# Optimization experiments

Measured on AMD Instinct MI355X. Metric: run time of the kernel, lower is better.

## Reference

```python
import jax, jax.numpy as jnp
import numpy as np

WH, WW = 7, 7           # window height/width
N = WH * WW             # tokens per window = 49
C = 768                 # num_channels
H = 24                  # num_heads
D = C // H              # head_dim = 32
B = 1024                # total windows (batch * windows-per-image)
NW = 64                 # windows per image (shift_mask leading dim)
EPS = 1e-5


def _relative_position_index():
    # Mirrors the torch buffer construction in __init__.
    coords = np.stack(np.meshgrid(np.arange(WH), np.arange(WW), indexing='ij'))  # [2,WH,WW]
    cf = coords.reshape(2, -1)                          # [2,N]
    rel = cf[:, :, None] - cf[:, None, :]               # [2,N,N]
    rel = rel.transpose(1, 2, 0).copy()                 # [N,N,2]
    rel[:, :, 0] += WH - 1
    rel[:, :, 1] += WW - 1
    rel[:, :, 0] *= 2 * WW - 1
    return jnp.asarray(rel.sum(-1), dtype=jnp.int32)    # [N,N]


def setup_inputs() -> dict:
    key = jax.random.key(0)
    ks = jax.random.split(key, 6)
    x = jax.random.normal(ks[0], (B, N, C), dtype=jnp.float32)
    shift_mask = jax.random.normal(ks[1], (NW, N, N), dtype=jnp.float32)
    w_qkv = jax.random.normal(ks[2], (3 * C, C), dtype=jnp.float32) * 0.02
    b_qkv = jnp.zeros((3 * C,), dtype=jnp.float32)
    w_proj = jax.random.normal(ks[3], (C, C), dtype=jnp.float32) * 0.02
    b_proj = jnp.zeros((C,), dtype=jnp.float32)
    rel_bias_table = jax.random.normal(ks[4], ((2 * WH - 1) * (2 * WW - 1), H), dtype=jnp.float32) * 0.02
    ln_g = jnp.ones((C,), dtype=jnp.float32)
    ln_b = jnp.zeros((C,), dtype=jnp.float32)
    rel_pos_index = _relative_position_index()
    return {
        'x': x, 'shift_mask': shift_mask,
        'w_qkv': w_qkv, 'b_qkv': b_qkv,
        'w_proj': w_proj, 'b_proj': b_proj,
        'rel_bias_table': rel_bias_table,
        'ln_g': ln_g, 'ln_b': ln_b,
        'rel_pos_index': rel_pos_index,
    }


def reference(x, shift_mask, w_qkv, b_qkv, w_proj, b_proj, rel_bias_table, ln_g, ln_b, rel_pos_index):
    B_, N_, C_ = x.shape
    # QKV projection: [B,N,3C] -> [3,B,H,N,D]
    qkv = (x @ w_qkv.T + b_qkv).reshape(B_, N_, 3, H, D).transpose(2, 0, 3, 1, 4)
    q, k, v = qkv[0], qkv[1], qkv[2]
    # Relative position bias gather: [N,N,H] -> [1,H,N,N]
    bias = rel_bias_table[rel_pos_index.reshape(-1)].reshape(N_, N_, H).transpose(2, 0, 1)[None]
    # Shift mask broadcast over batch repeats and heads: [B,1,N,N]
    mask = jnp.tile(shift_mask, (B_ // shift_mask.shape[0], 1, 1))[:, None]
    attn_bias = bias + mask  # [B,H,N,N]
    scale = 1.0 / np.sqrt(D).astype(np.float32)
    scores = jnp.einsum('bhnd,bhmd->bhnm', q, k) * scale + attn_bias
    attn = jax.nn.softmax(scores, axis=-1)
    out = jnp.einsum('bhnm,bhmd->bhnd', attn, v)       # [B,H,N,D]
    out = out.transpose(0, 2, 1, 3).reshape(B_, N_, C_)
    out = out @ w_proj.T + b_proj                      # dropout p=0 -> identity
    y = out + x
    mu = jnp.mean(y, axis=-1, keepdims=True)
    var = jnp.mean(jnp.square(y - mu), axis=-1, keepdims=True)
    return (y - mu) * jax.lax.rsqrt(var + EPS) * ln_g + ln_b
```

## Files before the change

### kernel.cpp

```cpp
#include <hip/hip_runtime.h>
#include <hip/hip_bf16.h>

#define SEQ 49
#define CH 768
#define NH 24
#define HD 32
#define NB 1024
#define NWIN 64
#define MTOT (NB*SEQ)

typedef __hip_bfloat16 bf16;
typedef __attribute__((ext_vector_type(8))) short short8;
typedef __attribute__((ext_vector_type(4))) short short4v;
typedef __attribute__((ext_vector_type(4))) float f32x4;

#define MD  ((size_t)MTOT * HD)
#define NHMD ((size_t)NH * MD)

__device__ __forceinline__ void gload16(const void* g, void* l) {
  __builtin_amdgcn_global_load_lds((__attribute__((address_space(1))) void*)g,
                                   (__attribute__((address_space(3))) void*)l,
                                   16, 0, 0);
}

__device__ __forceinline__ float bf2f(short s) {
  return __uint_as_float(((unsigned int)(unsigned short)s) << 16);
}

__global__ void cvt_bf16(const float* __restrict__ in, bf16* __restrict__ o, int n4) {
  int i = blockIdx.x * blockDim.x + threadIdx.x;
  if (i >= n4) return;
  float4 v = ((const float4*)in)[i];
  union { bf16 b[4]; short4 s; } u;
  u.b[0] = __float2bfloat16(v.x);
  u.b[1] = __float2bfloat16(v.y);
  u.b[2] = __float2bfloat16(v.z);
  u.b[3] = __float2bfloat16(v.w);
  ((short4*)o)[i] = u.s;
}

__global__ void build_comb(const float* __restrict__ table, const int* __restrict__ rpi,
                           const float* __restrict__ smask, bf16* __restrict__ comb) {
  int i = blockIdx.x * blockDim.x + threadIdx.x;
  if (i >= NWIN * NH * 1024) return;
  int idx = i * 4;
  int e0 = idx & 7;
  int l = (idx >> 3) & 63;
  int jj = (idx >> 9) & 7;
  int sh = idx >> 12;
  int h = sh % NH;
  int s = sh / NH;
  union { bf16 b[4]; short4 v; } u;
#pragma unroll
  for (int k = 0; k < 4; k++) {
    int j = jj * 8 + e0 + k;
    int mt = j >> 4, nt = (j >> 2) & 3, r = j & 3;
    int m = 16 * mt + 4 * (l >> 4) + r;
    int n = 16 * nt + (l & 15);
    float v = -1e30f;
    if (m < SEQ && n < SEQ)
      v = (table[rpi[m * SEQ + n] * NH + h] + smask[s * SEQ * SEQ + m * SEQ + n])
          * 1.4426950408889634f;
    u.b[k] = __float2bfloat16(v);
  }
  *(short4*)(comb + idx) = u.v;
}

__global__ __launch_bounds__(512) void qkv_gemm(
    const bf16* __restrict__ A, const bf16* __restrict__ Bw,
    const float* __restrict__ bias, bf16* __restrict__ C)
{
  extern __shared__ __align__(16) bf16 lds[];
  const int tid = threadIdx.x;
  const int w = tid >> 6, l = tid & 63;
  const int lr = l & 15, lg = l >> 4;
  const int wm = w >> 2, wn = w & 3;

  const int flat = blockIdx.x;
  const int xcd = flat & 7, lid = flat >> 3;
  const int wgid = (xcd < 4 ? xcd * 221 : 884 + (xcd - 4) * 220) + lid;
  const int bm = wgid / 9, bn = wgid - 9 * bm;

  const bf16* gA[4];
  const bf16* gB[4];
  int ldst[4];
#pragma unroll
  for (int j = 0; j < 4; j++) {
    int c = j * 512 + tid;
    int row = c >> 3, cpos = c & 7;
    int srcch = cpos ^ (row & 7);
    gA[j] = A + ((size_t)(bm * 256 + row)) * CH + srcch * 8;
    gB[j] = Bw + ((size_t)(bn * 256 + row)) * CH + srcch * 8;
    ldst[j] = c * 8;
  }

  f32x4 acc[8][4];
  f32x4 zero4 = {0.f, 0.f, 0.f, 0.f};
#pragma unroll
  for (int i = 0; i < 8; i++)
#pragma unroll
    for (int j = 0; j < 4; j++) acc[i][j] = zero4;

  int offA[8][2], offB[4][2];
#pragma unroll
  for (int mi = 0; mi < 8; mi++)
#pragma unroll
    for (int ks = 0; ks < 2; ks++) {
      int rowa = wm * 128 + mi * 16 + lr;
      offA[mi][ks] = rowa * 64 + ((lg + 4 * ks) ^ (rowa & 7)) * 8;
    }
#pragma unroll
  for (int nj = 0; nj < 4; nj++)
#pragma unroll
    for (int ks = 0; ks < 2; ks++) {
      int rowb = wn * 64 + nj * 16 + lr;
      offB[nj][ks] = rowb * 64 + ((lg + 4 * ks) ^ (rowb & 7)) * 8;
    }

#pragma unroll
  for (int j = 0; j < 4; j++) gload16(gA[j], lds + ldst[j]);
#pragma unroll
  for (int j = 0; j < 4; j++) gload16(gB[j], lds + 32768 + ldst[j]);

  for (int t = 0; t < 12; ++t) {
    const int cur = t & 1;
    asm volatile("s_waitcnt vmcnt(0)" ::: "memory");
    __builtin_amdgcn_sched_barrier(0);
    __builtin_amdgcn_s_barrier();
    __builtin_amdgcn_sched_barrier(0);
    const bf16* cA = lds + cur * 16384;
    const bf16* cB = lds + 32768 + cur * 16384;
    bf16* nA = lds + (cur ^ 1) * 16384;
    bf16* nB = lds + 32768 + (cur ^ 1) * 16384;
    const int kk = (t + 1) * 64;
    const bool pf = (t < 11);
#pragma unroll
    for (int ks = 0; ks < 2; ks++) {
      short8 bfv[4];
#pragma unroll
      for (int nj = 0; nj < 4; nj++) bfv[nj] = *(const short8*)(cB + offB[nj][ks]);
#pragma unroll
      for (int hp = 0; hp < 2; hp++) {
        short8 af[4];
#pragma unroll
        for (int mi = 0; mi < 4; mi++) af[mi] = *(const short8*)(cA + offA[hp * 4 + mi][ks]);
        if (pf) {
          const int j = ks * 2 + hp;
          gload16(gA[j] + kk, nA + ldst[j]);
          gload16(gB[j] + kk, nB + ldst[j]);
        }
        asm volatile("s_waitcnt lgkmcnt(0)" ::: "memory");
        __builtin_amdgcn_sched_barrier(0);
        __builtin_amdgcn_s_setprio(1);
#pragma unroll
        for (int mi = 0; mi < 4; mi++)
#pragma unroll
          for (int nj = 0; nj < 4; nj++)
            acc[hp * 4 + mi][nj] =
                __builtin_amdgcn_mfma_f32_16x16x32_bf16(af[mi], bfv[nj], acc[hp * 4 + mi][nj], 0, 0, 0);
        __builtin_amdgcn_s_setprio(0);
      }
    }
  }

  const float scale = 0.25503487724583985f;
  const int colbase = bn * 256 + 64 * wn;
  const int rowbase = bm * 256 + 128 * wm;
#pragma unroll
  for (int nj = 0; nj < 4; nj++) {
    const int cb16 = colbase + 16 * nj;
    const int sec = cb16 / 768;
    const int rem = cb16 - sec * 768;
    const int h = rem >> 5;
    const int dbase = rem & 31;
    float bv = bias[cb16 + lr];
    if (sec == 2) {
      const size_t vbase = 2 * NHMD + ((size_t)h * HD + dbase + lr) * MTOT;
#pragma unroll
      for (int mi = 0; mi < 8; mi++) {
        size_t row = rowbase + 16 * mi + 4 * lg;
        union { bf16 b[4]; short4 s; } u;
#pragma unroll
        for (int r = 0; r < 4; r++) u.b[r] = __float2bfloat16(acc[mi][nj][r] + bv);
        *(short4*)(C + vbase + row) = u.s;
      }
    } else {
      const float mul = (sec == 0) ? scale : 1.0f;
      const size_t base = (size_t)sec * NHMD + (size_t)h * MD + dbase + lr;
#pragma unroll
      for (int mi = 0; mi < 8; mi++) {
#pragma unroll
        for (int r = 0; r < 4; r++) {
          size_t row = rowbase + 16 * mi + 4 * lg + r;
          C[base + row * HD] = __float2bfloat16((acc[mi][nj][r] + bv) * mul);
        }
      }
    }
  }
}

__global__ __launch_bounds__(256, 3) void attn_kernel(
    const bf16* __restrict__ qkvT, const bf16* __restrict__ comb,
    bf16* __restrict__ aout)
{
  __shared__ __align__(16) bf16 P[4][64 * 72];
  const int tid = threadIdx.x;
  const int w = tid >> 6, l = tid & 63;
  const int lr = l & 15, lg = l >> 4;
  const int b = blockIdx.x;
  const int h = blockIdx.y * 4 + w;
  const size_t rowb = (size_t)b * SEQ;
  f32x4 zero4 = {0.f, 0.f, 0.f, 0.f};

  const bf16* qb = qkvT + (size_t)h * MD + rowb * HD;
  const bf16* kb = qkvT + NHMD + (size_t)h * MD + rowb * HD;
  const bf16* vT = qkvT + 2 * NHMD + (size_t)h * HD * MTOT;

  short8 qf[4], kf[4];
#pragma unroll
  for (int mt = 0; mt < 4; mt++)
    qf[mt] = *(const short8*)(qb + (16 * mt + lr) * HD + 8 * lg);
#pragma unroll
  for (int nt = 0; nt < 4; nt++)
    kf[nt] = *(const short8*)(kb + (16 * nt + lr) * HD + 8 * lg);

  f32x4 s[4][4];
#pragma unroll
  for (int mt = 0; mt < 4; mt++)
#pragma unroll
    for (int nt = 0; nt < 4; nt++)
      s[mt][nt] = __builtin_amdgcn_mfma_f32_16x16x32_bf16(qf[mt], kf[nt], zero4, 0, 0, 0);

  short8 pb[2][2];
#pragma unroll
  for (int kt = 0; kt < 2; kt++)
#pragma unroll
    for (int dt = 0; dt < 2; dt++)
      pb[kt][dt] = *(const short8*)(vT + ((size_t)(16 * dt + lr)) * MTOT + rowb + 32 * kt + 8 * lg);

  const bf16* cbp = comb + (((size_t)(b & (NWIN - 1)) * NH + h) << 12);
  short8 c8[8];
#pragma unroll
  for (int jj = 0; jj < 8; jj++)
    c8[jj] = *(const short8*)(cbp + (jj * 64 + l) * 8);
#pragma unroll
  for (int jj = 0; jj < 8; jj++)
#pragma unroll
    for (int e = 0; e < 8; e++)
      s[jj >> 1][(jj & 1) * 2 + (e >> 2)][e & 3] += bf2f(c8[jj][e]);

  float inv[4][4];
#pragma unroll
  for (int mt = 0; mt < 4; mt++)
#pragma unroll
    for (int r = 0; r < 4; r++) {
      float t = 0.f;
#pragma unroll
      for (int nt = 0; nt < 4; nt++) {
        float e = exp2f(s[mt][nt][r]);
        s[mt][nt][r] = e;
        t += e;
      }
      t += __shfl_xor(t, 1, 64);
      t += __shfl_xor(t, 2, 64);
      t += __shfl_xor(t, 4, 64);
      t += __shfl_xor(t, 8, 64);
      inv[mt][r] = 1.0f / t;
    }

#pragma unroll
  for (int mt = 0; mt < 4; mt++)
#pragma unroll
    for (int nt = 0; nt < 4; nt++)
#pragma unroll
      for (int r = 0; r < 4; r++)
        P[w][(16 * mt + 4 * lg + r) * 72 + 16 * nt + lr] =
            __float2bfloat16(s[mt][nt][r]);

  f32x4 o[4][2];
#pragma unroll
  for (int mt = 0; mt < 4; mt++) { o[mt][0] = zero4; o[mt][1] = zero4; }
#pragma unroll
  for (int kt = 0; kt < 2; kt++) {
    short8 pa[4];
#pragma unroll
    for (int mt = 0; mt < 4; mt++)
      pa[mt] = *(const short8*)(&P[w][(16 * mt + lr) * 72 + 32 * kt + 8 * lg]);
#pragma unroll
    for (int mt = 0; mt < 4; mt++)
#pragma unroll
      for (int dt = 0; dt < 2; dt++)
        o[mt][dt] = __builtin_amdgcn_mfma_f32_16x16x32_bf16(pa[mt], pb[kt][dt], o[mt][dt], 0, 0, 0);
  }

#pragma unroll
  for (int mt = 0; mt < 4; mt++)
#pragma unroll
    for (int dt = 0; dt < 2; dt++)
#pragma unroll
      for (int r = 0; r < 4; r++) {
        int m = 16 * mt + 4 * lg + r;
        if (m < SEQ)
          aout[(rowb + m) * CH + h * HD + 16 * dt + lr] =
              __float2bfloat16(o[mt][dt][r] * inv[mt][r]);
      }
}

__global__ __launch_bounds__(256) void proj_gemm(
    const bf16* __restrict__ A, const bf16* __restrict__ Bw,
    const float* __restrict__ bias, const bf16* __restrict__ xb,
    bf16* __restrict__ Y)
{
  __shared__ __align__(16) bf16 As[2 * 128 * 64];
  __shared__ __align__(16) bf16 Bs[2 * 128 * 64];
  const int tid = threadIdx.x;
  const int w = tid >> 6, l = tid & 63;
  const int lr = l & 15, lg = l >> 4;
  const int wm = w >> 1, wn = w & 1;

  const int flat = blockIdx.x;
  const int wg = (flat & 7) * 294 + (flat >> 3);
  const int bm = wg / 6, bn = wg - 6 * (wg / 6);

  const bf16* gA[4];
  const bf16* gB[4];
  int ldst[4];
#pragma unroll
  for (int j = 0; j < 4; j++) {
    int c = j * 256 + tid;
    int row = c >> 3, cpos = c & 7;
    int srcch = cpos ^ (row & 7);
    gA[j] = A + ((size_t)(bm * 128 + row)) * CH + srcch * 8;
    gB[j] = Bw + ((size_t)(bn * 128 + row)) * CH + srcch * 8;
    ldst[j] = c * 8;
  }

  f32x4 acc[4][4];
  f32x4 zero4 = {0.f, 0.f, 0.f, 0.f};
#pragma unroll
  for (int i = 0; i < 4; i++)
#pragma unroll
    for (int j = 0; j < 4; j++) acc[i][j] = zero4;

  int offA[4][2], offB[4][2];
#pragma unroll
  for (int mi = 0; mi < 4; mi++) {
#pragma unroll
    for (int ks = 0; ks < 2; ks++) {
      int rowa = 64 * wm + 16 * mi + lr;
      offA[mi][ks] = rowa * 64 + ((lg + 4 * ks) ^ (rowa & 7)) * 8;
      int rowb = 64 * wn + 16 * mi + lr;
      offB[mi][ks] = rowb * 64 + ((lg + 4 * ks) ^ (rowb & 7)) * 8;
    }
  }

#pragma unroll
  for (int j = 0; j < 4; j++) gload16(gA[j], As + ldst[j]);
#pragma unroll
  for (int j = 0; j < 4; j++) gload16(gB[j], Bs + ldst[j]);

  for (int t = 0; t < 12; ++t) {
    const int base = (t & 1) * 8192;
    asm volatile("s_waitcnt vmcnt(0)" ::: "memory");
    __builtin_amdgcn_sched_barrier(0);
    __builtin_amdgcn_s_barrier();
    __builtin_amdgcn_sched_barrier(0);
    const bf16* cA = As + base;
    const bf16* cB = Bs + base;
    bf16* nA = As + (base ^ 8192);
    bf16* nB = Bs + (base ^ 8192);
    const int kk = (t + 1) * 64;
    const bool pf = (t < 11);
#pragma unroll
    for (int ks = 0; ks < 2; ks++) {
      short8 af[4], bfv[4];
#pragma unroll
      for (int mi = 0; mi < 4; mi++) {
        af[mi] = *(const short8*)(cA + offA[mi][ks]);
        bfv[mi] = *(const short8*)(cB + offB[mi][ks]);
      }
      if (pf) {
#pragma unroll
        for (int j = 0; j < 2; j++) {
          gload16(gA[ks * 2 + j] + kk, nA + ldst[ks * 2 + j]);
          gload16(gB[ks * 2 + j] + kk, nB + ldst[ks * 2 + j]);
        }
      }
      asm volatile("s_waitcnt lgkmcnt(0)" ::: "memory");
      __builtin_amdgcn_sched_barrier(0);
      __builtin_amdgcn_s_setprio(1);
#pragma unroll
      for (int mi = 0; mi < 4; mi++)
#pragma unroll
        for (int nj = 0; nj < 4; nj++)
          acc[mi][nj] = __builtin_amdgcn_mfma_f32_16x16x32_bf16(af[mi], bfv[nj], acc[mi][nj], 0, 0, 0);
      __builtin_amdgcn_s_setprio(0);
    }
  }

  const int colbase = bn * 128 + 64 * wn;
  const int rowbase = bm * 128 + 64 * wm;
#pragma unroll
  for (int nj = 0; nj < 4; nj++) {
    int col = colbase + 16 * nj + lr;
    float bv = bias[col];
#pragma unroll
    for (int mi = 0; mi < 4; mi++) {
#pragma unroll
      for (int r = 0; r < 4; r++) {
        size_t row = rowbase + 16 * mi + 4 * lg + r;
        float v = acc[mi][nj][r] + bv + bf2f(((const short*)xb)[row * CH + col]);
        Y[row * CH + col] = __float2bfloat16(v);
      }
    }
  }
}

__global__ __launch_bounds__(256) void ln_kernel(
    const bf16* __restrict__ Y, const float* __restrict__ g,
    const float* __restrict__ be, float* __restrict__ out)
{
  const int w = threadIdx.x >> 6, l = threadIdx.x & 63;
  const size_t r = (size_t)blockIdx.x * 4 + w;
  const bf16* yr = Y + r * CH;

  short8 a = *(const short8*)(yr + 8 * l);
  short4v b4 = *(const short4v*)(yr + 512 + 4 * l);
  float v[12];
#pragma unroll
  for (int j = 0; j < 8; j++) v[j] = bf2f(a[j]);
#pragma unroll
  for (int j = 0; j < 4; j++) v[8 + j] = bf2f(b4[j]);

  float s1 = 0.f, s2 = 0.f;
#pragma unroll
  for (int j = 0; j < 12; j++) { s1 += v[j]; s2 += v[j] * v[j]; }
#pragma unroll
  for (int m = 1; m <= 32; m <<= 1) {
    s1 += __shfl_xor(s1, m, 64);
    s2 += __shfl_xor(s2, m, 64);
  }
  float mu = s1 * (1.0f / 768.0f);
  float var = s2 * (1.0f / 768.0f) - mu * mu;
  float rs = rsqrtf(var + 1e-5f);

  float4 g0 = *(const float4*)(g + 8 * l);
  float4 g1 = *(const float4*)(g + 8 * l + 4);
  float4 g2 = *(const float4*)(g + 512 + 4 * l);
  float4 b0 = *(const float4*)(be + 8 * l);
  float4 b1 = *(const float4*)(be + 8 * l + 4);
  float4 b2 = *(const float4*)(be + 512 + 4 * l);

  float4 o0, o1, o2;
  o0.x = (v[0] - mu) * rs * g0.x + b0.x;
  o0.y = (v[1] - mu) * rs * g0.y + b0.y;
  o0.z = (v[2] - mu) * rs * g0.z + b0.z;
  o0.w = (v[3] - mu) * rs * g0.w + b0.w;
  o1.x = (v[4] - mu) * rs * g1.x + b1.x;
  o1.y = (v[5] - mu) * rs * g1.y + b1.y;
  o1.z = (v[6] - mu) * rs * g1.z + b1.z;
  o1.w = (v[7] - mu) * rs * g1.w + b1.w;
  o2.x = (v[8] - mu) * rs * g2.x + b2.x;
  o2.y = (v[9] - mu) * rs * g2.y + b2.y;
  o2.z = (v[10] - mu) * rs * g2.z + b2.z;
  o2.w = (v[11] - mu) * rs * g2.w + b2.w;

  float* orow = out + r * CH;
  *(float4*)(orow + 8 * l) = o0;
  *(float4*)(orow + 8 * l + 4) = o1;
  *(float4*)(orow + 512 + 4 * l) = o2;
}

extern "C" void kernel_launch(void* const* d_in, const int* in_sizes, int n_in,
                              void* d_out, int out_size, void* d_ws, size_t ws_size,
                              hipStream_t stream) {
  (void)in_sizes; (void)n_in; (void)out_size; (void)ws_size;
  const float* x     = (const float*)d_in[0];
  const float* smask = (const float*)d_in[1];
  const float* wqkv  = (const float*)d_in[2];
  const float* bqkv  = (const float*)d_in[3];
  const float* wproj = (const float*)d_in[4];
  const float* bproj = (const float*)d_in[5];
  const float* table = (const float*)d_in[6];
  const float* lng   = (const float*)d_in[7];
  const float* lnb   = (const float*)d_in[8];
  const int*   rpi   = (const int*)d_in[9];
  float* out = (float*)d_out;

  char* ws = (char*)d_ws;
  bf16*  xb   = (bf16*)(ws);
  bf16*  wqb  = (bf16*)(ws + 77070336);
  bf16*  wpb  = (bf16*)(ws + 80609280);
  bf16*  comb = (bf16*)(ws + 81788928);
  bf16*  qkvT = (bf16*)(ws + 94371840);
  bf16*  aout = (bf16*)(ws + 325582848);
  bf16*  yb   = (bf16*)(ws + 94371840);

  cvt_bf16<<<37632, 256, 0, stream>>>(x, xb, 9633792);
  cvt_bf16<<<1728, 256, 0, stream>>>(wqkv, wqb, 442368);
  cvt_bf16<<<576, 256, 0, stream>>>(wproj, wpb, 147456);
  build_comb<<<6144, 256, 0, stream>>>(table, rpi, smask, comb);
  qkv_gemm<<<1764, 512, 131072, stream>>>(xb, wqb, bqkv, qkvT);
  attn_kernel<<<dim3(1024, 6), 256, 0, stream>>>(qkvT, comb, aout);
  proj_gemm<<<2352, 256, 0, stream>>>(aout, wpb, bproj, xb, yb);
  ln_kernel<<<12544, 256, 0, stream>>>(yb, lng, lnb, out);
}
```

Baseline: 540.8 us.

## Split QKV GEMM k-tile wait into staged partial vmcnt waits per quarter

Reorders the global-to-LDS prefetch so B tiles and then A row-halves are issued in the order they are consumed. Each k-tile is now split into four phases, each gated by a partial vmcnt wait and a workgroup barrier, in place of one full vmcnt(0) wait at the top of the tile. The goal is to start MFMA work on the first arrived chunks while later loads are still in flight. The cost is four barriers per k-tile instead of one, and correctness now relies on the exact vmcnt counts matching the load issue order.

```diff
diff --git a/kernel.cpp b/kernel.cpp
--- a/kernel.cpp
+++ b/kernel.cpp
@@ -117,17 +117,17 @@
       offB[nj][ks] = rowb * 64 + ((lg + 4 * ks) ^ (rowb & 7)) * 8;
     }
 
-#pragma unroll
-  for (int j = 0; j < 4; j++) gload16(gA[j], lds + ldst[j]);
-#pragma unroll
-  for (int j = 0; j < 4; j++) gload16(gB[j], lds + 32768 + ldst[j]);
+  gload16(gB[0], lds + 32768 + ldst[0]);
+  gload16(gB[1], lds + 32768 + ldst[1]);
+  gload16(gB[2], lds + 32768 + ldst[2]);
+  gload16(gB[3], lds + 32768 + ldst[3]);
+  gload16(gA[0], lds + ldst[0]);
+  gload16(gA[2], lds + ldst[2]);
+  gload16(gA[1], lds + ldst[1]);
+  gload16(gA[3], lds + ldst[3]);
 
   for (int t = 0; t < 12; ++t) {
     const int cur = t & 1;
-    asm volatile("s_waitcnt vmcnt(0)" ::: "memory");
-    __builtin_amdgcn_sched_barrier(0);
-    __builtin_amdgcn_s_barrier();
-    __builtin_amdgcn_sched_barrier(0);
     const bf16* cA = lds + cur * 16384;
     const bf16* cB = lds + 32768 + cur * 16384;
     bf16* nA = lds + (cur ^ 1) * 16384;
@@ -135,31 +135,38 @@
     const int kk = (t + 1) * 64;
     const bool pf = (t < 11);
 #pragma unroll
-    for (int ks = 0; ks < 2; ks++) {
-      short8 bfv[4];
+    for (int p = 0; p < 4; ++p) {
+      const int hp = p >> 1, ks = p & 1;
+      if (p == 0) {
+        asm volatile("s_waitcnt vmcnt(2)" ::: "memory");
+      } else if (p == 2) {
+        if (pf) asm volatile("s_waitcnt vmcnt(4)" ::: "memory");
+        else    asm volatile("s_waitcnt vmcnt(0)" ::: "memory");
+      }
+      __builtin_amdgcn_sched_barrier(0);
+      __builtin_amdgcn_s_barrier();
+      __builtin_amdgcn_sched_barrier(0);
+      short8 af[4], bfv[4];
+#pragma unroll
+      for (int mi = 0; mi < 4; mi++) af[mi] = *(const short8*)(cA + offA[hp * 4 + mi][ks]);
 #pragma unroll
       for (int nj = 0; nj < 4; nj++) bfv[nj] = *(const short8*)(cB + offB[nj][ks]);
-#pragma unroll
-      for (int hp = 0; hp < 2; hp++) {
-        short8 af[4];
-#pragma unroll
-        for (int mi = 0; mi < 4; mi++) af[mi] = *(const short8*)(cA + offA[hp * 4 + mi][ks]);
-        if (pf) {
-          const int j = ks * 2 + hp;
-          gload16(gA[j] + kk, nA + ldst[j]);
-          gload16(gB[j] + kk, nB + ldst[j]);
-        }
-        asm volatile("s_waitcnt lgkmcnt(0)" ::: "memory");
-        __builtin_amdgcn_sched_barrier(0);
-        __builtin_amdgcn_s_setprio(1);
-#pragma unroll
-        for (int mi = 0; mi < 4; mi++)
-#pragma unroll
-          for (int nj = 0; nj < 4; nj++)
-            acc[hp * 4 + mi][nj] =
-                __builtin_amdgcn_mfma_f32_16x16x32_bf16(af[mi], bfv[nj], acc[hp * 4 + mi][nj], 0, 0, 0);
-        __builtin_amdgcn_s_setprio(0);
-      }
+      if (pf) {
+        if (p == 0) { gload16(gB[0] + kk, nB + ldst[0]); gload16(gB[1] + kk, nB + ldst[1]); }
+        if (p == 1) { gload16(gB[2] + kk, nB + ldst[2]); gload16(gB[3] + kk, nB + ldst[3]); }
+        if (p == 2) { gload16(gA[0] + kk, nA + ldst[0]); gload16(gA[2] + kk, nA + ldst[2]); }
+        if (p == 3) { gload16(gA[1] + kk, nA + ldst[1]); gload16(gA[3] + kk, nA + ldst[3]); }
+      }
+      asm volatile("s_waitcnt lgkmcnt(0)" ::: "memory");
+      __builtin_amdgcn_sched_barrier(0);
+      __builtin_amdgcn_s_setprio(1);
+#pragma unroll
+      for (int mi = 0; mi < 4; mi++)
+#pragma unroll
+        for (int nj = 0; nj < 4; nj++)
+          acc[hp * 4 + mi][nj] =
+              __builtin_amdgcn_mfma_f32_16x16x32_bf16(af[mi], bfv[nj], acc[hp * 4 + mi][nj], 0, 0, 0);
+      __builtin_amdgcn_s_setprio(0);
     }
   }
 
```

Measured after the change: 520.3 us. -3.8%, faster.
